# Kernel optimization log

Measured on AMD Instinct MI355X. Metric: run time of the kernel, lower is better.

## Reference

```python
import jax, jax.numpy as jnp
import numpy as np

N_LETTERS = 128
WORD_DIM = 128      # word embed dim; char-LSTM hidden = 64 per direction
SENT_DIM = 256      # sentence embed dim; word-LSTM hidden = 128 per direction
B, S, LW = 128, 64, 16


def _lstm_dir(x, Wih, Whh, b, reverse):
    """One direction of an LSTM. x: [B,T,D], Wih: [4H,D], Whh: [4H,H], b: [4H].
    PyTorch gate order (i, f, g, o). Returns (outputs [B,T,H], final h [B,H])."""
    Bc = x.shape[0]
    H = Whh.shape[-1]
    xw = jnp.einsum('btd,gd->btg', x, Wih) + b  # precompute input projections

    def step(carry, xt):
        h, c = carry
        g = xt + h @ Whh.T
        i, f, gg, o = jnp.split(g, 4, axis=-1)
        c = jax.nn.sigmoid(f) * c + jax.nn.sigmoid(i) * jnp.tanh(gg)
        h = jax.nn.sigmoid(o) * jnp.tanh(c)
        return (h, c), h

    z = jnp.zeros((Bc, H), x.dtype)
    (h, _), hs = jax.lax.scan(step, (z, z), jnp.swapaxes(xw, 0, 1), reverse=reverse)
    return jnp.swapaxes(hs, 0, 1), h


def _bilstm_final(x, Wih_per_layer, Whh, b):
    """2-layer bidirectional LSTM; returns concat of last-layer final hiddens [B,2H].
    Wih_per_layer: list of length 2 of [2,4H,Din_l]; Whh: [2,2,4H,H]; b: [2,2,4H]."""
    hf = hb = None
    for l in range(2):
        of, hf = _lstm_dir(x, Wih_per_layer[l][0], Whh[l, 0], b[l, 0], False)
        ob, hb = _lstm_dir(x, Wih_per_layer[l][1], Whh[l, 1], b[l, 1], True)
        x = jnp.concatenate([of, ob], axis=-1)
    return jnp.concatenate([hf, hb], axis=-1)


def _mlp2(h, W1, b1, W2, b2):
    return jax.nn.relu(h @ W1.T + b1) @ W2.T + b2


def setup_inputs() -> dict:
    rng = np.random.default_rng(0)
    # sentences: non-empty words contiguous at the front of each sentence
    sent_lens = rng.integers(8, S + 1, B)
    word_lens = rng.integers(1, LW + 1, (B, S))
    chars = rng.integers(1, N_LETTERS + 1, (B, S, LW))
    pos = np.arange(LW)
    chars = np.where(pos[None, None, :] < word_lens[:, :, None], chars, 0)
    chars = np.where(np.arange(S)[None, :, None] < sent_lens[:, None, None], chars, 0)
    sentences = jnp.asarray(chars, dtype=jnp.int32)
    # target words: all non-empty (filter in WordEmbedder is then identity)
    wlens = rng.integers(1, LW + 1, B)
    wchars = rng.integers(1, N_LETTERS + 1, (B, LW))
    wchars = np.where(pos[None, :] < wlens[:, None], wchars, 0)
    words = jnp.asarray(wchars, dtype=jnp.int32)

    ks = jax.random.split(jax.random.key(0), 32)
    sc = 0.05
    Hw, Hs = WORD_DIM // 2, SENT_DIM // 2  # 64, 128
    p = {
        'sentences': sentences, 'words': words,
        'emb': jax.random.normal(ks[0], (N_LETTERS + 1, WORD_DIM)) * sc,
        # char-level word LSTM: both layers have input dim WORD_DIM
        'w_Wih': jax.random.normal(ks[1], (2, 2, 4 * Hw, WORD_DIM)) * sc,
        'w_Whh': jax.random.normal(ks[2], (2, 2, 4 * Hw, Hw)) * sc,
        'w_b': jax.random.normal(ks[3], (2, 2, 4 * Hw)) * sc,
        'w_fc_W1': jax.random.normal(ks[4], (WORD_DIM, WORD_DIM)) * sc,
        'w_fc_b1': jax.random.normal(ks[5], (WORD_DIM,)) * sc,
        'w_fc_W2': jax.random.normal(ks[6], (WORD_DIM, WORD_DIM)) * sc,
        'w_fc_b2': jax.random.normal(ks[7], (WORD_DIM,)) * sc,
        # sentence LSTM: layer0 input WORD_DIM, layer1 input SENT_DIM
        's_Wih0': jax.random.normal(ks[8], (2, 4 * Hs, WORD_DIM)) * sc,
        's_Wih1': jax.random.normal(ks[9], (2, 4 * Hs, SENT_DIM)) * sc,
        's_Whh': jax.random.normal(ks[10], (2, 2, 4 * Hs, Hs)) * sc,
        's_b': jax.random.normal(ks[11], (2, 2, 4 * Hs)) * sc,
        's_fc_W1': jax.random.normal(ks[12], (SENT_DIM, SENT_DIM)) * sc,
        's_fc_b1': jax.random.normal(ks[13], (SENT_DIM,)) * sc,
        's_fc_W2': jax.random.normal(ks[14], (SENT_DIM, SENT_DIM)) * sc,
        's_fc_b2': jax.random.normal(ks[15], (SENT_DIM,)) * sc,
        # classifier 384 -> 256 -> 128 -> 2
        'c_W0': jax.random.normal(ks[16], (256, SENT_DIM + WORD_DIM)) * sc,
        'c_b0': jax.random.normal(ks[17], (256,)) * sc,
        'c_W1': jax.random.normal(ks[18], (128, 256)) * sc,
        'c_b1': jax.random.normal(ks[19], (128,)) * sc,
        'c_W2': jax.random.normal(ks[20], (2, 128)) * sc,
        'c_b2': jax.random.normal(ks[21], (2,)) * sc,
    }
    return p


def _word_embed(tokens, emb, w_Wih, w_Whh, w_b, W1, b1, W2, b2):
    x = emb[tokens]  # [N, LW, WORD_DIM]
    h = _bilstm_final(x, [w_Wih[0], w_Wih[1]], w_Whh, w_b)
    return _mlp2(h, W1, b1, W2, b2)


def reference(sentences, words, emb, w_Wih, w_Whh, w_b, w_fc_W1, w_fc_b1,
              w_fc_W2, w_fc_b2, s_Wih0, s_Wih1, s_Whh, s_b, s_fc_W1, s_fc_b1,
              s_fc_W2, s_fc_b2, c_W0, c_b0, c_W1, c_b1, c_W2, c_b2):
    Bc, Sc, Lc = sentences.shape
    flat = sentences.reshape(-1, Lc)
    we = _word_embed(flat, emb, w_Wih, w_Whh, w_b,
                     w_fc_W1, w_fc_b1, w_fc_W2, w_fc_b2)  # [B*S, WORD_DIM]
    # ragged scatter-pad == zero-mask empty word slots (non-empty words are at front)
    nonempty = (flat != 0).any(axis=1)  # [B*S]
    unflat = (we * nonempty[:, None].astype(we.dtype)).reshape(Bc, Sc, WORD_DIM)
    hs = _bilstm_final(unflat, [s_Wih0, s_Wih1], s_Whh, s_b)
    sent_emb = _mlp2(hs, s_fc_W1, s_fc_b1, s_fc_W2, s_fc_b2)  # [B, SENT_DIM]
    word_emb = _word_embed(words, emb, w_Wih, w_Whh, w_b,
                           w_fc_W1, w_fc_b1, w_fc_W2, w_fc_b2)  # [B, WORD_DIM]
    x = jnp.concatenate([sent_emb, word_emb], axis=1)
    x = jax.nn.relu(x @ c_W0.T + c_b0)
    x = jax.nn.relu(x @ c_W1.T + c_b1)
    x = x @ c_W2.T + c_b2
    return jax.nn.log_softmax(x, axis=1)
```

## Files before the change

### kernel.cpp

```cpp
#include <hip/hip_runtime.h>
#include <hip/hip_bf16.h>
#include <math.h>

typedef unsigned int u32;
typedef unsigned short u16;
typedef unsigned long long u64;
typedef __hip_bfloat16 bf16_t;
typedef float f32x4 __attribute__((ext_vector_type(4)));
typedef short bf16x8 __attribute__((ext_vector_type(8)));

__device__ __forceinline__ float blo(u32 p){ union{u32 u; float f;} c; c.u = p << 16; return c.f; }
__device__ __forceinline__ float bhi(u32 p){ union{u32 u; float f;} c; c.u = p & 0xFFFF0000u; return c.f; }
#define LOG2E  1.44269504088896340736f
#define LOG2E2 2.88539008177792681472f
__device__ __forceinline__ float fsigm(float x){
  return __builtin_amdgcn_rcpf(1.0f + __builtin_amdgcn_exp2f(-x*LOG2E));
}
__device__ __forceinline__ float ftanh(float x){
  return 1.0f - 2.0f*__builtin_amdgcn_rcpf(1.0f + __builtin_amdgcn_exp2f(x*LOG2E2));
}
__device__ __forceinline__ u16 f2bu(float f){
  union{float f; u32 u;} c; c.f = f;
  u32 u = c.u + 0x7FFFu + ((c.u >> 16) & 1u);
  return (u16)(u >> 16);
}

#define WE_OFF   0u
#define L0O_OFF  2129920u
#define SFIN_OFF 6324224u
#define XW_OFF   6455296u
#define WB_OFF   40009728u
#define SEG_WWIH  0
#define SEG_WWHH  131072
#define SEG_FW1   196608
#define SEG_FW2   212992
#define SEG_SWIH0 229376
#define SEG_SWIH1 360448
#define SEG_SWHH  622592
#define SEG_TOTAL 884736
#define EMB_TOTAL 16512

__global__ __launch_bounds__(256) void prep_weights(
    const float* __restrict__ wWih, const float* __restrict__ wWhh,
    const float* __restrict__ fW1,  const float* __restrict__ fW2,
    const float* __restrict__ sWih0,const float* __restrict__ sWih1,
    const float* __restrict__ sWhh, const float* __restrict__ emb,
    u16* __restrict__ dst, u16* __restrict__ embB)
{
  for (int i = blockIdx.x*256 + threadIdx.x; i < SEG_TOTAL + EMB_TOTAL; i += gridDim.x*256){
    if (i < SEG_TOTAL){
      const float* s; int off;
      if      (i < SEG_WWHH ){ s = wWih;  off = i; }
      else if (i < SEG_FW1  ){ s = wWhh;  off = i - SEG_WWHH; }
      else if (i < SEG_FW2  ){ s = fW1;   off = i - SEG_FW1; }
      else if (i < SEG_SWIH0){ s = fW2;   off = i - SEG_FW2; }
      else if (i < SEG_SWIH1){ s = sWih0; off = i - SEG_SWIH0; }
      else if (i < SEG_SWHH ){ s = sWih1; off = i - SEG_SWIH1; }
      else                   { s = sWhh;  off = i - SEG_SWHH; }
      dst[i] = f2bu(s[off]);
    } else {
      embB[i - SEG_TOTAL] = f2bu(emb[i - SEG_TOTAL]);
    }
  }
}

__global__ __launch_bounds__(512, 2) void word_mfma(
    const int* __restrict__ sentences, const int* __restrict__ words,
    const u16* __restrict__ embB,
    const u16* __restrict__ wWihB, const u16* __restrict__ wWhhB,
    const float* __restrict__ wb,
    const u16* __restrict__ fW1B, const float* __restrict__ fb1,
    const u16* __restrict__ fW2B, const float* __restrict__ fb2,
    bf16_t* __restrict__ we_out )
{
  const int blk  = blockIdx.x;
  const int tid  = threadIdx.x;
  const int lane = tid & 63;
  const int wv   = tid >> 6;
  const int dq   = wv >> 2;
  const int wq   = wv & 3;
  const int lr   = lane & 15;
  const int lg   = lane >> 4;

  __shared__ __align__(16) u16 SQ[16*16*128];
  __shared__ __align__(16) u16 Hb[2][2][16*64];
  __shared__ __align__(16) u16 HF[16*128];
  __shared__ int chs[256];
  __shared__ int emptyf[16];
  u16* A1 = (u16*)Hb;

  const int wbase = blk*16;
  if (tid < 256){
    int w = tid >> 4, t = tid & 15;
    int gw = wbase + w;
    chs[tid] = (gw < 8192) ? sentences[gw*16 + t] : words[(gw - 8192)*16 + t];
  }
  __syncthreads();
  if (tid < 16){
    int acc = 0;
    #pragma unroll
    for (int i = 0; i < 16; ++i) acc |= chs[tid*16 + i];
    emptyf[tid] = (wbase + tid < 8192) && (acc == 0);
  }
  __syncthreads();

  {
    int allz = 1;
    #pragma unroll
    for (int i = 0; i < 16; ++i) allz &= emptyf[i];
    if (allz){
      u64* wo = (u64*)(we_out + (size_t)wbase*128);
      wo[tid] = 0ull;
      return;
    }
  }

  for (int layer = 0; layer < 2; ++layer){
    const int ld = layer*2 + dq;
    bf16x8 bih[4][4], bhh[4][2];
    float bias[4];
    #pragma unroll
    for (int j = 0; j < 4; ++j){
      const int col = (wq + 4*j)*16 + lr;
      bias[j] = wb[ld*256 + col];
      const u16* pih = wWihB + (size_t)(ld*256 + col)*128 + lg*8;
      #pragma unroll
      for (int kk = 0; kk < 4; ++kk) bih[j][kk] = *(const bf16x8*)(pih + kk*32);
      const u16* phh = wWhhB + (size_t)(ld*256 + col)*64 + lg*8;
      #pragma unroll
      for (int kk = 0; kk < 2; ++kk) bhh[j][kk] = *(const bf16x8*)(phh + kk*32);
    }
    float cst[4] = {0.f, 0.f, 0.f, 0.f};
    for (int i = tid; i < 2*2*16*64; i += 512) ((u16*)Hb)[i] = 0;
    __syncthreads();
    int cur = 0;
    bf16x8 xfn[4];
    if (layer == 0){
      const int t0 = dq ? 15 : 0;
      const u16* xp = embB + (size_t)chs[lr*16 + t0]*128 + lg*8;
      #pragma unroll
      for (int kk = 0; kk < 4; ++kk) xfn[kk] = *(const bf16x8*)(xp + kk*32);
    }
    for (int step = 0; step < 16; ++step){
      const int t = dq ? (15 - step) : step;
      f32x4 ac[4];
      #pragma unroll
      for (int j = 0; j < 4; ++j) ac[j] = (f32x4){bias[j], bias[j], bias[j], bias[j]};
      if (layer == 0){
        bf16x8 xf[4];
        #pragma unroll
        for (int kk = 0; kk < 4; ++kk) xf[kk] = xfn[kk];
        if (step < 15){
          const int tn = dq ? (14 - step) : (step + 1);
          const u16* xp = embB + (size_t)chs[lr*16 + tn]*128 + lg*8;
          #pragma unroll
          for (int kk = 0; kk < 4; ++kk) xfn[kk] = *(const bf16x8*)(xp + kk*32);
        }
        #pragma unroll
        for (int kk = 0; kk < 4; ++kk){
          #pragma unroll
          for (int j = 0; j < 4; ++j)
            ac[j] = __builtin_amdgcn_mfma_f32_16x16x32_bf16(xf[kk], bih[j][kk], ac[j], 0, 0, 0);
        }
      } else {
        #pragma unroll
        for (int kk = 0; kk < 4; ++kk){
          const int c = (kk*4 + lg) ^ lr;
          bf16x8 a = *(const bf16x8*)&SQ[((lr*16 + t)*16 + c)*8];
          #pragma unroll
          for (int j = 0; j < 4; ++j)
            ac[j] = __builtin_amdgcn_mfma_f32_16x16x32_bf16(a, bih[j][kk], ac[j], 0, 0, 0);
        }
      }
      #pragma unroll
      for (int kk = 0; kk < 2; ++kk){
        const int c = (kk*4 + lg) ^ (lr & 7);
        bf16x8 a = *(const bf16x8*)&Hb[dq][cur][(lr*8 + c)*8];
        #pragma unroll
        for (int j = 0; j < 4; ++j)
          ac[j] = __builtin_amdgcn_mfma_f32_16x16x32_bf16(a, bhh[j][kk], ac[j], 0, 0, 0);
      }
      const int u = wq*16 + lr;
      #pragma unroll
      for (int r = 0; r < 4; ++r){
        const int w = lg*4 + r;
        float ig = fsigm(ac[0][r]);
        float fg = fsigm(ac[1][r]);
        float gg = ftanh(ac[2][r]);
        float og = fsigm(ac[3][r]);
        cst[r] = fg*cst[r] + ig*gg;
        float hn = og * ftanh(cst[r]);
        u16 hb = f2bu(hn);
        Hb[dq][cur^1][(w*8 + ((u >> 3) ^ (w & 7)))*8 + (u & 7)] = hb;
        const int d = dq*64 + u;
        const int dc = (d >> 3) ^ (w & 15);
        if (layer == 0)       SQ[((w*16 + t)*16 + dc)*8 + (d & 7)] = hb;
        else if (step == 15)  HF[(w*16 + dc)*8 + (d & 7)] = hb;
      }
      __syncthreads();
      cur ^= 1;
    }
  }

  {
    const int col = wv*16 + lr;
    float bs = fb1[col];
    bf16x8 b1[4];
    const u16* src = fW1B + (size_t)col*128 + lg*8;
    #pragma unroll
    for (int kk = 0; kk < 4; ++kk) b1[kk] = *(const bf16x8*)(src + kk*32);
    f32x4 ac = (f32x4){bs, bs, bs, bs};
    #pragma unroll
    for (int kk = 0; kk < 4; ++kk){
      const int c = (kk*4 + lg) ^ lr;
      bf16x8 a = *(const bf16x8*)&HF[(lr*16 + c)*8];
      ac = __builtin_amdgcn_mfma_f32_16x16x32_bf16(a, b1[kk], ac, 0, 0, 0);
    }
    __syncthreads();
    #pragma unroll
    for (int r = 0; r < 4; ++r){
      const int w = lg*4 + r;
      A1[(w*16 + ((col >> 3) ^ (w & 15)))*8 + (col & 7)] = f2bu(fmaxf(ac[r], 0.f));
    }
  }
  __syncthreads();
  {
    const int col = wv*16 + lr;
    float bs = fb2[col];
    bf16x8 b2[4];
    const u16* src = fW2B + (size_t)col*128 + lg*8;
    #pragma unroll
    for (int kk = 0; kk < 4; ++kk) b2[kk] = *(const bf16x8*)(src + kk*32);
    f32x4 ac = (f32x4){bs, bs, bs, bs};
    #pragma unroll
    for (int kk = 0; kk < 4; ++kk){
      const int c = (kk*4 + lg) ^ lr;
      bf16x8 a = *(const bf16x8*)&A1[(lr*16 + c)*8];
      ac = __builtin_amdgcn_mfma_f32_16x16x32_bf16(a, b2[kk], ac, 0, 0, 0);
    }
    u16* wo = (u16*)we_out;
    #pragma unroll
    for (int r = 0; r < 4; ++r){
      const int w = lg*4 + r;
      wo[(size_t)(wbase + w)*128 + col] = emptyf[w] ? (u16)0 : f2bu(ac[r]);
    }
  }
}

template<int KK>
__global__ __launch_bounds__(256, 1) void xw_gemm(
    const u16* __restrict__ X, const u16* __restrict__ W,
    const float* __restrict__ bias, float* __restrict__ out)
{
  const int rowb = blockIdx.x;
  const int colb = blockIdx.y;
  const int tid = threadIdx.x;
  const int lane = tid & 63, wv = tid >> 6;
  const int lr = lane & 15, lg = lane >> 4;
  const int K = KK*32;

  bf16x8 bf[4][KK];
  f32x4 ac[4];
  #pragma unroll
  for (int j = 0; j < 4; ++j){
    const int g = colb*256 + (wv*4 + j)*16 + lr;
    const float bs = bias[g];
    ac[j] = (f32x4){bs, bs, bs, bs};
    const u16* src = W + (size_t)g*K + lg*8;
    #pragma unroll
    for (int kk = 0; kk < KK; ++kk) bf[j][kk] = *(const bf16x8*)(src + kk*32);
  }
  const u16* xr = X + (size_t)(rowb*16 + lr)*K + lg*8;
  #pragma unroll
  for (int kk = 0; kk < KK; ++kk){
    bf16x8 a = *(const bf16x8*)(xr + kk*32);
    #pragma unroll
    for (int j = 0; j < 4; ++j)
      ac[j] = __builtin_amdgcn_mfma_f32_16x16x32_bf16(a, bf[j][kk], ac[j], 0, 0, 0);
  }
  #pragma unroll
  for (int j = 0; j < 4; ++j){
    const int g = colb*256 + (wv*4 + j)*16 + lr;
    #pragma unroll
    for (int r = 0; r < 4; ++r)
      out[(size_t)(rowb*16 + lg*4 + r)*1024 + g] = ac[j][r];
  }
}

__global__ __launch_bounds__(512, 1) void sent_rec(
    const float* __restrict__ xw ,
    const u16* __restrict__ sWhhB ,
    bf16_t* __restrict__ l0out ,
    float* __restrict__ sfin ,
    const int layer)
{
  const int dir = blockIdx.x & 1;
  const int sg0 = (blockIdx.x >> 1) << 4;
  const int tid = threadIdx.x;
  const int lane = tid & 63, wv = tid >> 6;
  const int lr = lane & 15, lg = lane >> 4;

  __shared__ __align__(16) u16 Hs[2][2048];

  bf16x8 bhh[4][4];
  #pragma unroll
  for (int j = 0; j < 4; ++j){
    const int g = (wv + 8*j)*16 + lr;
    const u16* p = sWhhB + (size_t)((layer*2 + dir)*512 + g)*128 + lg*8;
    #pragma unroll
    for (int kk = 0; kk < 4; ++kk) bhh[j][kk] = *(const bf16x8*)(p + kk*32);
  }
  for (int i = tid; i < 4096; i += 512) ((u16*)Hs)[i] = 0;
  float cst[4] = {0.f, 0.f, 0.f, 0.f};

  const float* xb[4];
  #pragma unroll
  for (int r = 0; r < 4; ++r)
    xb[r] = xw + (size_t)(sg0 + lg*4 + r)*64*1024 + dir*512 + wv*16 + lr;
  const int u = wv*16 + lr;
  u16* lob = (u16*)l0out;
  __syncthreads();

  int cur = 0;
  for (int g8 = 0; g8 < 8; ++g8){
    const int s0 = g8*8;
    float xws[8][16];
    #pragma unroll
    for (int s8 = 0; s8 < 8; ++s8){
      const int t = dir ? (63 - (s0 + s8)) : (s0 + s8);
      #pragma unroll
      for (int j = 0; j < 4; ++j)
        #pragma unroll
        for (int r = 0; r < 4; ++r)
          xws[s8][j*4 + r] = xb[r][(size_t)t*1024 + j*128];
    }
    u16 hs8[8][4];
    #pragma unroll
    for (int s8 = 0; s8 < 8; ++s8){
      f32x4 ac[4];
      #pragma unroll
      for (int j = 0; j < 4; ++j)
        ac[j] = (f32x4){xws[s8][j*4+0], xws[s8][j*4+1], xws[s8][j*4+2], xws[s8][j*4+3]};
      #pragma unroll
      for (int kk = 0; kk < 4; ++kk){
        const bf16x8 ha = *(const bf16x8*)&Hs[cur][(lr*16 + ((kk*4 + lg) ^ lr))*8];
        #pragma unroll
        for (int j = 0; j < 4; ++j)
          ac[j] = __builtin_amdgcn_mfma_f32_16x16x32_bf16(ha, bhh[j][kk], ac[j], 0, 0, 0);
      }
      #pragma unroll
      for (int r = 0; r < 4; ++r){
        const int s = lg*4 + r;
        float ig = fsigm(ac[0][r]);
        float fg = fsigm(ac[1][r]);
        float gg = ftanh(ac[2][r]);
        float og = fsigm(ac[3][r]);
        cst[r] = fg*cst[r] + ig*gg;
        float hn = og * ftanh(cst[r]);
        u16 hb = f2bu(hn);
        hs8[s8][r] = hb;
        Hs[cur^1][(s*16 + ((u >> 3) ^ s))*8 + (u & 7)] = hb;
        if (layer == 1 && (s0 + s8) == 63)
          sfin[(size_t)(sg0 + s)*256 + dir*128 + u] = hn;
      }
      __syncthreads();
      cur ^= 1;
    }
    if (layer == 0){
      #pragma unroll
      for (int s8 = 0; s8 < 8; ++s8){
        const int t = dir ? (63 - (s0 + s8)) : (s0 + s8);
        #pragma unroll
        for (int r = 0; r < 4; ++r){
          const int s = lg*4 + r;
          lob[((size_t)(sg0 + s)*64 + t)*256 + dir*128 + u] = hs8[s8][r];
        }
      }
    }
  }
}

__global__ __launch_bounds__(256) void head_kernel(
    const float* __restrict__ sfin, const bf16_t* __restrict__ wet,
    const float* __restrict__ sW1, const float* __restrict__ sb1,
    const float* __restrict__ sW2, const float* __restrict__ sb2,
    const float* __restrict__ cW0, const float* __restrict__ cb0,
    const float* __restrict__ cW1, const float* __restrict__ cb1,
    const float* __restrict__ cW2, const float* __restrict__ cb2,
    float* __restrict__ out)
{
  const int bs = blockIdx.x, tid = threadIdx.x;
  __shared__ __align__(16) float hin[256];
  __shared__ __align__(16) float a1[256];
  __shared__ __align__(16) float xcat[384];
  __shared__ __align__(16) float b0o[256];
  __shared__ __align__(16) float h1o[128];
  __shared__ float lg[2];

  hin[tid] = sfin[(size_t)bs*256 + tid];
  if (tid < 64){
    const u32* src = (const u32*)(wet + (size_t)bs*128);
    u32 p = src[tid];
    xcat[256 + tid*2]     = blo(p);
    xcat[256 + tid*2 + 1] = bhi(p);
  }
  __syncthreads();
  {
    const float4* wr = (const float4*)(sW1 + (size_t)tid*256);
    float acc = sb1[tid];
    #pragma unroll
    for (int i = 0; i < 64; ++i){
      float4 v = wr[i]; const float* hp = &hin[i*4];
      acc += hp[0]*v.x + hp[1]*v.y + hp[2]*v.z + hp[3]*v.w;
    }
    a1[tid] = fmaxf(acc, 0.0f);
  }
  __syncthreads();
  {
    const float4* wr = (const float4*)(sW2 + (size_t)tid*256);
    float acc = sb2[tid];
    #pragma unroll
    for (int i = 0; i < 64; ++i){
      float4 v = wr[i]; const float* hp = &a1[i*4];
      acc += hp[0]*v.x + hp[1]*v.y + hp[2]*v.z + hp[3]*v.w;
    }
    xcat[tid] = acc;
  }
  __syncthreads();
  {
    const float4* wr = (const float4*)(cW0 + (size_t)tid*384);
    float acc = cb0[tid];
    #pragma unroll
    for (int i = 0; i < 96; ++i){
      float4 v = wr[i]; const float* hp = &xcat[i*4];
      acc += hp[0]*v.x + hp[1]*v.y + hp[2]*v.z + hp[3]*v.w;
    }
    b0o[tid] = fmaxf(acc, 0.0f);
  }
  __syncthreads();
  if (tid < 128){
    const float4* wr = (const float4*)(cW1 + (size_t)tid*256);
    float acc = cb1[tid];
    #pragma unroll
    for (int i = 0; i < 64; ++i){
      float4 v = wr[i]; const float* hp = &b0o[i*4];
      acc += hp[0]*v.x + hp[1]*v.y + hp[2]*v.z + hp[3]*v.w;
    }
    h1o[tid] = fmaxf(acc, 0.0f);
  }
  __syncthreads();
  if (tid < 2){
    const float4* wr = (const float4*)(cW2 + (size_t)tid*128);
    float acc = cb2[tid];
    #pragma unroll
    for (int i = 0; i < 32; ++i){
      float4 v = wr[i]; const float* hp = &h1o[i*4];
      acc += hp[0]*v.x + hp[1]*v.y + hp[2]*v.z + hp[3]*v.w;
    }
    lg[tid] = acc;
  }
  __syncthreads();
  if (tid == 0){
    float m = fmaxf(lg[0], lg[1]);
    float lse = m + logf(expf(lg[0] - m) + expf(lg[1] - m));
    out[bs*2 + 0] = lg[0] - lse;
    out[bs*2 + 1] = lg[1] - lse;
  }
}

extern "C" void kernel_launch(void* const* d_in, const int* in_sizes, int n_in,
                              void* d_out, int out_size, void* d_ws, size_t ws_size,
                              hipStream_t stream) {
  const int*   sentences = (const int*)d_in[0];
  const int*   words     = (const int*)d_in[1];
  const float* emb    = (const float*)d_in[2];
  const float* wWih   = (const float*)d_in[3];
  const float* wWhh   = (const float*)d_in[4];
  const float* wb     = (const float*)d_in[5];
  const float* fW1    = (const float*)d_in[6];
  const float* fb1    = (const float*)d_in[7];
  const float* fW2    = (const float*)d_in[8];
  const float* fb2    = (const float*)d_in[9];
  const float* sWih0  = (const float*)d_in[10];
  const float* sWih1  = (const float*)d_in[11];
  const float* sWhh   = (const float*)d_in[12];
  const float* sb     = (const float*)d_in[13];
  const float* sW1    = (const float*)d_in[14];
  const float* sb1    = (const float*)d_in[15];
  const float* sW2    = (const float*)d_in[16];
  const float* sb2    = (const float*)d_in[17];
  const float* cW0    = (const float*)d_in[18];
  const float* cb0    = (const float*)d_in[19];
  const float* cW1    = (const float*)d_in[20];
  const float* cb1    = (const float*)d_in[21];
  const float* cW2    = (const float*)d_in[22];
  const float* cb2    = (const float*)d_in[23];

  char* W = (char*)d_ws;
  bf16_t* we   = (bf16_t*)(W + WE_OFF);
  bf16_t* l0o  = (bf16_t*)(W + L0O_OFF);
  float*  sfin = (float*) (W + SFIN_OFF);
  float*  xw   = (float*) (W + XW_OFF);
  u16*    embB = (u16*)   (W + XW_OFF);
  u16*    wB   = (u16*)   (W + WB_OFF);
  bf16_t* wet  = we + (size_t)8192*128;

  prep_weights<<<dim3(440), dim3(256), 0, stream>>>(
      wWih, wWhh, fW1, fW2, sWih0, sWih1, sWhh, emb, wB, embB);
  word_mfma<<<dim3(520), dim3(512), 0, stream>>>(
      sentences, words, embB,
      wB + SEG_WWIH, wB + SEG_WWHH, wb,
      wB + SEG_FW1, fb1, wB + SEG_FW2, fb2, we);
  xw_gemm<4><<<dim3(512, 4), dim3(256), 0, stream>>>(
      (const u16*)we, wB + SEG_SWIH0, sb, xw);
  sent_rec<<<dim3(16), dim3(512), 0, stream>>>(xw, wB + SEG_SWHH, l0o, sfin, 0);
  xw_gemm<8><<<dim3(512, 4), dim3(256), 0, stream>>>(
      (const u16*)l0o, wB + SEG_SWIH1, sb + 1024, xw);
  sent_rec<<<dim3(16), dim3(512), 0, stream>>>(xw, wB + SEG_SWHH, l0o, sfin, 1);
  head_kernel<<<dim3(128), dim3(256), 0, stream>>>(
      sfin, wet, sW1, sb1, sW2, sb2, cW0, cb0, cW1, cb1, cW2, cb2,
      (float*)d_out);
}
```

Before: 405.3 us.

## Fuse sentence-LSTM input projection GEMMs into the recurrent kernels

Result: slower. 467.8 us (+15.4%).

```diff
diff --git a/kernel.cpp b/kernel.cpp
--- a/kernel.cpp
+++ b/kernel.cpp
@@ -28,7 +28,7 @@
 #define WE_OFF   0u
 #define L0O_OFF  2129920u
 #define SFIN_OFF 6324224u
-#define XW_OFF   6455296u
+#define EMB_OFF  6455296u
 #define WB_OFF   40009728u
 #define SEG_WWIH  0
 #define SEG_WWHH  131072
@@ -247,52 +247,11 @@
   }
 }
 
-template<int KK>
-__global__ __launch_bounds__(256, 1) void xw_gemm(
-    const u16* __restrict__ X, const u16* __restrict__ W,
-    const float* __restrict__ bias, float* __restrict__ out)
-{
-  const int rowb = blockIdx.x;
-  const int colb = blockIdx.y;
-  const int tid = threadIdx.x;
-  const int lane = tid & 63, wv = tid >> 6;
-  const int lr = lane & 15, lg = lane >> 4;
-  const int K = KK*32;
-
-  bf16x8 bf[4][KK];
-  f32x4 ac[4];
-  #pragma unroll
-  for (int j = 0; j < 4; ++j){
-    const int g = colb*256 + (wv*4 + j)*16 + lr;
-    const float bs = bias[g];
-    ac[j] = (f32x4){bs, bs, bs, bs};
-    const u16* src = W + (size_t)g*K + lg*8;
-    #pragma unroll
-    for (int kk = 0; kk < KK; ++kk) bf[j][kk] = *(const bf16x8*)(src + kk*32);
-  }
-  const u16* xr = X + (size_t)(rowb*16 + lr)*K + lg*8;
-  #pragma unroll
-  for (int kk = 0; kk < KK; ++kk){
-    bf16x8 a = *(const bf16x8*)(xr + kk*32);
-    #pragma unroll
-    for (int j = 0; j < 4; ++j)
-      ac[j] = __builtin_amdgcn_mfma_f32_16x16x32_bf16(a, bf[j][kk], ac[j], 0, 0, 0);
-  }
-  #pragma unroll
-  for (int j = 0; j < 4; ++j){
-    const int g = colb*256 + (wv*4 + j)*16 + lr;
-    #pragma unroll
-    for (int r = 0; r < 4; ++r)
-      out[(size_t)(rowb*16 + lg*4 + r)*1024 + g] = ac[j][r];
-  }
-}
-
-__global__ __launch_bounds__(512, 1) void sent_rec(
-    const float* __restrict__ xw ,
-    const u16* __restrict__ sWhhB ,
-    bf16_t* __restrict__ l0out ,
-    float* __restrict__ sfin ,
-    const int layer)
+__global__ __launch_bounds__(512, 1) void sent_l0_mfma(
+    const u16* __restrict__ we ,
+    const u16* __restrict__ sWih0B, const u16* __restrict__ sWhhB,
+    const float* __restrict__ sb,
+    bf16_t* __restrict__ l0out )
 {
   const int dir = blockIdx.x & 1;
   const int sg0 = (blockIdx.x >> 1) << 4;
@@ -302,81 +261,158 @@
 
   __shared__ __align__(16) u16 Hs[2][2048];
 
-  bf16x8 bhh[4][4];
+  bf16x8 bih[4][4], bhh[4][4];
+  float bias[4];
   #pragma unroll
   for (int j = 0; j < 4; ++j){
     const int g = (wv + 8*j)*16 + lr;
-    const u16* p = sWhhB + (size_t)((layer*2 + dir)*512 + g)*128 + lg*8;
-    #pragma unroll
-    for (int kk = 0; kk < 4; ++kk) bhh[j][kk] = *(const bf16x8*)(p + kk*32);
+    bias[j] = sb[dir*512 + g];
+    const u16* pih = sWih0B + (size_t)(dir*512 + g)*128 + lg*8;
+    const u16* phh = sWhhB  + (size_t)(dir*512 + g)*128 + lg*8;
+    #pragma unroll
+    for (int kk = 0; kk < 4; ++kk){
+      bih[j][kk] = *(const bf16x8*)(pih + kk*32);
+      bhh[j][kk] = *(const bf16x8*)(phh + kk*32);
+    }
   }
   for (int i = tid; i < 4096; i += 512) ((u16*)Hs)[i] = 0;
   float cst[4] = {0.f, 0.f, 0.f, 0.f};
-
-  const float* xb[4];
+  __syncthreads();
+
+  const u16* xbase = we + (size_t)(sg0 + lr)*64*128 + lg*8;
+  u16* lob = (u16*)l0out;
+  int cur = 0;
+  bf16x8 xfn[4];
+  {
+    const int t0 = dir ? 63 : 0;
+    const u16* xr = xbase + (size_t)t0*128;
+    #pragma unroll
+    for (int kk = 0; kk < 4; ++kk) xfn[kk] = *(const bf16x8*)(xr + kk*32);
+  }
+  for (int step = 0; step < 64; ++step){
+    const int t = dir ? (63 - step) : step;
+    bf16x8 xf[4];
+    #pragma unroll
+    for (int kk = 0; kk < 4; ++kk) xf[kk] = xfn[kk];
+    if (step < 63){
+      const int tn = dir ? (62 - step) : (step + 1);
+      const u16* xr = xbase + (size_t)tn*128;
+      #pragma unroll
+      for (int kk = 0; kk < 4; ++kk) xfn[kk] = *(const bf16x8*)(xr + kk*32);
+    }
+    f32x4 ac[4];
+    #pragma unroll
+    for (int j = 0; j < 4; ++j) ac[j] = (f32x4){bias[j], bias[j], bias[j], bias[j]};
+    #pragma unroll
+    for (int kk = 0; kk < 4; ++kk){
+      const bf16x8 ha = *(const bf16x8*)&Hs[cur][(lr*16 + ((kk*4 + lg) ^ lr))*8];
+      #pragma unroll
+      for (int j = 0; j < 4; ++j)
+        ac[j] = __builtin_amdgcn_mfma_f32_16x16x32_bf16(ha, bhh[j][kk], ac[j], 0, 0, 0);
+    }
+    #pragma unroll
+    for (int kk = 0; kk < 4; ++kk){
+      #pragma unroll
+      for (int j = 0; j < 4; ++j)
+        ac[j] = __builtin_amdgcn_mfma_f32_16x16x32_bf16(xf[kk], bih[j][kk], ac[j], 0, 0, 0);
+    }
+    const int u = wv*16 + lr;
+    #pragma unroll
+    for (int r = 0; r < 4; ++r){
+      const int s = lg*4 + r;
+      float ig = fsigm(ac[0][r]);
+      float fg = fsigm(ac[1][r]);
+      float gg = ftanh(ac[2][r]);
+      float og = fsigm(ac[3][r]);
+      cst[r] = fg*cst[r] + ig*gg;
+      float hn = og * ftanh(cst[r]);
+      u16 hb = f2bu(hn);
+      Hs[cur^1][(s*16 + ((u >> 3) ^ s))*8 + (u & 7)] = hb;
+      lob[((size_t)(sg0 + s)*64 + t)*256 + dir*128 + u] = hb;
+    }
+    __syncthreads();
+    cur ^= 1;
+  }
+}
+
+__global__ __launch_bounds__(512, 1) void sent_l1_mfma(
+    const u16* __restrict__ l0out ,
+    const u16* __restrict__ sWih1B, const u16* __restrict__ sWhhB,
+    const float* __restrict__ sb,
+    float* __restrict__ sfin )
+{
+  const int dir = blockIdx.x & 1;
+  const int sg0 = (blockIdx.x >> 1) << 4;
+  const int tid = threadIdx.x;
+  const int lane = tid & 63, wv = tid >> 6;
+  const int lr = lane & 15, lg = lane >> 4;
+
+  __shared__ __align__(16) u16 Hs[2][2048];
+
+  bf16x8 bih[4][8], bhh[4][4];
+  float bias[4];
   #pragma unroll
-  for (int r = 0; r < 4; ++r)
-    xb[r] = xw + (size_t)(sg0 + lg*4 + r)*64*1024 + dir*512 + wv*16 + lr;
-  const int u = wv*16 + lr;
-  u16* lob = (u16*)l0out;
-  __syncthreads();
-
+  for (int j = 0; j < 4; ++j){
+    const int g = (wv + 8*j)*16 + lr;
+    bias[j] = sb[(2 + dir)*512 + g];
+    const u16* pih = sWih1B + (size_t)(dir*512 + g)*256 + lg*8;
+    const u16* phh = sWhhB  + (size_t)((2 + dir)*512 + g)*128 + lg*8;
+    #pragma unroll
+    for (int kk = 0; kk < 8; ++kk) bih[j][kk] = *(const bf16x8*)(pih + kk*32);
+    #pragma unroll
+    for (int kk = 0; kk < 4; ++kk) bhh[j][kk] = *(const bf16x8*)(phh + kk*32);
+  }
+  for (int i = tid; i < 4096; i += 512) ((u16*)Hs)[i] = 0;
+  float cst[4] = {0.f, 0.f, 0.f, 0.f};
+  __syncthreads();
+
+  const u16* xbase = l0out + (size_t)(sg0 + lr)*64*256 + lg*8;
   int cur = 0;
-  for (int g8 = 0; g8 < 8; ++g8){
-    const int s0 = g8*8;
-    float xws[8][16];
-    #pragma unroll
-    for (int s8 = 0; s8 < 8; ++s8){
-      const int t = dir ? (63 - (s0 + s8)) : (s0 + s8);
+  for (int step = 0; step < 64; ++step){
+    const int t = dir ? (63 - step) : step;
+    const u16* xr = xbase + (size_t)t*256;
+    f32x4 ac[4];
+    #pragma unroll
+    for (int j = 0; j < 4; ++j) ac[j] = (f32x4){bias[j], bias[j], bias[j], bias[j]};
+    bf16x8 xf[4];
+    #pragma unroll
+    for (int kk = 0; kk < 4; ++kk) xf[kk] = *(const bf16x8*)(xr + kk*32);
+    #pragma unroll
+    for (int kk = 0; kk < 4; ++kk){
+      const bf16x8 ha = *(const bf16x8*)&Hs[cur][(lr*16 + ((kk*4 + lg) ^ lr))*8];
       #pragma unroll
       for (int j = 0; j < 4; ++j)
-        #pragma unroll
-        for (int r = 0; r < 4; ++r)
-          xws[s8][j*4 + r] = xb[r][(size_t)t*1024 + j*128];
-    }
-    u16 hs8[8][4];
-    #pragma unroll
-    for (int s8 = 0; s8 < 8; ++s8){
-      f32x4 ac[4];
+        ac[j] = __builtin_amdgcn_mfma_f32_16x16x32_bf16(ha, bhh[j][kk], ac[j], 0, 0, 0);
+    }
+    #pragma unroll
+    for (int kk = 0; kk < 4; ++kk){
       #pragma unroll
       for (int j = 0; j < 4; ++j)
-        ac[j] = (f32x4){xws[s8][j*4+0], xws[s8][j*4+1], xws[s8][j*4+2], xws[s8][j*4+3]};
-      #pragma unroll
-      for (int kk = 0; kk < 4; ++kk){
-        const bf16x8 ha = *(const bf16x8*)&Hs[cur][(lr*16 + ((kk*4 + lg) ^ lr))*8];
-        #pragma unroll
-        for (int j = 0; j < 4; ++j)
-          ac[j] = __builtin_amdgcn_mfma_f32_16x16x32_bf16(ha, bhh[j][kk], ac[j], 0, 0, 0);
-      }
-      #pragma unroll
-      for (int r = 0; r < 4; ++r){
-        const int s = lg*4 + r;
-        float ig = fsigm(ac[0][r]);
-        float fg = fsigm(ac[1][r]);
-        float gg = ftanh(ac[2][r]);
-        float og = fsigm(ac[3][r]);
-        cst[r] = fg*cst[r] + ig*gg;
-        float hn = og * ftanh(cst[r]);
-        u16 hb = f2bu(hn);
-        hs8[s8][r] = hb;
-        Hs[cur^1][(s*16 + ((u >> 3) ^ s))*8 + (u & 7)] = hb;
-        if (layer == 1 && (s0 + s8) == 63)
-          sfin[(size_t)(sg0 + s)*256 + dir*128 + u] = hn;
-      }
-      __syncthreads();
-      cur ^= 1;
-    }
-    if (layer == 0){
-      #pragma unroll
-      for (int s8 = 0; s8 < 8; ++s8){
-        const int t = dir ? (63 - (s0 + s8)) : (s0 + s8);
-        #pragma unroll
-        for (int r = 0; r < 4; ++r){
-          const int s = lg*4 + r;
-          lob[((size_t)(sg0 + s)*64 + t)*256 + dir*128 + u] = hs8[s8][r];
-        }
-      }
-    }
+        ac[j] = __builtin_amdgcn_mfma_f32_16x16x32_bf16(xf[kk], bih[j][kk], ac[j], 0, 0, 0);
+    }
+    #pragma unroll
+    for (int kk = 0; kk < 4; ++kk) xf[kk] = *(const bf16x8*)(xr + 128 + kk*32);
+    #pragma unroll
+    for (int kk = 0; kk < 4; ++kk){
+      #pragma unroll
+      for (int j = 0; j < 4; ++j)
+        ac[j] = __builtin_amdgcn_mfma_f32_16x16x32_bf16(xf[kk], bih[j][4 + kk], ac[j], 0, 0, 0);
+    }
+    const int u = wv*16 + lr;
+    #pragma unroll
+    for (int r = 0; r < 4; ++r){
+      const int s = lg*4 + r;
+      float ig = fsigm(ac[0][r]);
+      float fg = fsigm(ac[1][r]);
+      float gg = ftanh(ac[2][r]);
+      float og = fsigm(ac[3][r]);
+      cst[r] = fg*cst[r] + ig*gg;
+      float hn = og * ftanh(cst[r]);
+      Hs[cur^1][(s*16 + ((u >> 3) ^ s))*8 + (u & 7)] = f2bu(hn);
+      if (step == 63) sfin[(size_t)(sg0 + s)*256 + dir*128 + u] = hn;
+    }
+    __syncthreads();
+    cur ^= 1;
   }
 }
 
@@ -500,8 +536,7 @@
   bf16_t* we   = (bf16_t*)(W + WE_OFF);
   bf16_t* l0o  = (bf16_t*)(W + L0O_OFF);
   float*  sfin = (float*) (W + SFIN_OFF);
-  float*  xw   = (float*) (W + XW_OFF);
-  u16*    embB = (u16*)   (W + XW_OFF);
+  u16*    embB = (u16*)   (W + EMB_OFF);
   u16*    wB   = (u16*)   (W + WB_OFF);
   bf16_t* wet  = we + (size_t)8192*128;
 
@@ -511,12 +546,10 @@
       sentences, words, embB,
       wB + SEG_WWIH, wB + SEG_WWHH, wb,
       wB + SEG_FW1, fb1, wB + SEG_FW2, fb2, we);
-  xw_gemm<4><<<dim3(512, 4), dim3(256), 0, stream>>>(
-      (const u16*)we, wB + SEG_SWIH0, sb, xw);
-  sent_rec<<<dim3(16), dim3(512), 0, stream>>>(xw, wB + SEG_SWHH, l0o, sfin, 0);
-  xw_gemm<8><<<dim3(512, 4), dim3(256), 0, stream>>>(
-      (const u16*)l0o, wB + SEG_SWIH1, sb + 1024, xw);
-  sent_rec<<<dim3(16), dim3(512), 0, stream>>>(xw, wB + SEG_SWHH, l0o, sfin, 1);
+  sent_l0_mfma<<<dim3(16), dim3(512), 0, stream>>>(
+      (const u16*)we, wB + SEG_SWIH0, wB + SEG_SWHH, sb, l0o);
+  sent_l1_mfma<<<dim3(16), dim3(512), 0, stream>>>(
+      (const u16*)l0o, wB + SEG_SWIH1, wB + SEG_SWHH, sb, sfin);
   head_kernel<<<dim3(128), dim3(256), 0, stream>>>(
       sfin, wet, sW1, sb1, sW2, sb2, cW0, cb0, cW1, cb1, cW2, cb2,
       (float*)d_out);
```
